# Kernel tuning notes

Measured on AMD Instinct MI355X. Metric: run time of the kernel, lower is better.

The kernel has to match this reference:

```python
import jax, jax.numpy as jnp
import numpy as np

EMB = 768
HEADS = 8
B, N = 8, 1024

def _ln(x, g, b, eps=1e-5):
    mu = jnp.mean(x, axis=-1, keepdims=True)
    var = jnp.mean(jnp.square(x - mu), axis=-1, keepdims=True)
    return (x - mu) * jax.lax.rsqrt(var + eps) * g + b

def setup_inputs() -> dict:
    key = jax.random.key(0)
    ks = jax.random.split(key, 8)
    s_in = 0.02
    return {
        "x": jax.random.normal(ks[0], (B, N, EMB), jnp.float32),
        "w_qkvr": jax.random.normal(ks[1], (EMB, 4 * EMB), jnp.float32) * s_in,
        "b_qkvr": jnp.zeros((4 * EMB,), jnp.float32),
        "w_proj": jax.random.normal(ks[2], (EMB, EMB), jnp.float32) * s_in,
        "b_proj": jnp.zeros((EMB,), jnp.float32),
        "ln1_g": jnp.ones((EMB,), jnp.float32),
        "ln1_b": jnp.zeros((EMB,), jnp.float32),
        "w_ff1": jax.random.normal(ks[3], (EMB, 4 * EMB), jnp.float32) * s_in,
        "b_ff1": jnp.zeros((4 * EMB,), jnp.float32),
        "w_ff2": jax.random.normal(ks[4], (4 * EMB, EMB), jnp.float32) * s_in,
        "b_ff2": jnp.zeros((EMB,), jnp.float32),
        "ln2_g": jnp.ones((EMB,), jnp.float32),
        "ln2_b": jnp.zeros((EMB,), jnp.float32),
    }

def reference(x, w_qkvr, b_qkvr, w_proj, b_proj, ln1_g, ln1_b,
              w_ff1, b_ff1, w_ff2, b_ff2, ln2_g, ln2_b):
    b, n, e = x.shape
    h = HEADS
    d = e // h
    # fused QKV+R projection; einops '(h d qkvr)' => qkvr is the INNERMOST factor
    qkvr = (x @ w_qkvr + b_qkvr).reshape(b, n, h, d, 4)
    qkvr = jnp.transpose(qkvr, (4, 0, 2, 1, 3))  # [4, b, h, n, d]
    q, k, v, r = qkvr[0], qkvr[1], qkvr[2], qkvr[3]
    energy = jnp.einsum('bhqd,bhkd->bhqk', q, k)
    # quirk: softmax of UNSCALED logits, then divide by sqrt(emb_size) AFTER
    att = jax.nn.softmax(energy, axis=-1) / jnp.sqrt(jnp.float32(e))
    out = jnp.einsum('bhqk,bhkd->bhqd', att, v)
    out = out * r  # elementwise r-gate
    out = jnp.transpose(out, (0, 2, 1, 3)).reshape(b, n, e)
    out = out @ w_proj + b_proj
    x1 = _ln(out + x, ln1_g, ln1_b)  # residual then post-LayerNorm
    ff = jax.nn.gelu(x1 @ w_ff1 + b_ff1, approximate=False) @ w_ff2 + b_ff2
    return _ln(ff + x1, ln2_g, ln2_b)
```

## Files before the change

kernel.cpp:

```cpp
#include <hip/hip_runtime.h>
#include <math.h>


typedef __bf16 bf16_t;
typedef __bf16 bf16x4 __attribute__((ext_vector_type(4)));
typedef __bf16 bf16x8 __attribute__((ext_vector_type(8)));
typedef float f32x4 __attribute__((ext_vector_type(4)));

#define EMB   768
#define HEADS 8
#define DHEAD 96
#define BATCH 8
#define SEQ   1024
#define ROWS  (BATCH * SEQ)
#define ACTN  ((size_t)ROWS * EMB)

__device__ __forceinline__ void load16_lds(const bf16_t* g, bf16_t* l) {
    __builtin_amdgcn_global_load_lds(
        (__attribute__((address_space(1))) unsigned int*)g,
        (__attribute__((address_space(3))) unsigned int*)l,
        16, 0, 0);
}


__device__ __forceinline__ void tile_transpose(
    const float* __restrict__ in, bf16_t* __restrict__ out,
    int K, int N, int n0, int k0, float (*t)[33], int tx, int ty0)
{
#pragma unroll
    for (int i = 0; i < 4; i++) {
        int ty = ty0 + 8 * i;
        t[ty][tx] = in[(size_t)(k0 + ty) * N + n0 + tx];
    }
    __syncthreads();
#pragma unroll
    for (int i = 0; i < 4; i++) {
        int ty = ty0 + 8 * i;
        out[(size_t)(n0 + ty) * K + k0 + tx] = (bf16_t)t[tx][ty];
    }
}

__global__ __launch_bounds__(256) void prep_kernel(
    const float* __restrict__ x, bf16_t* __restrict__ xb,
    const float* __restrict__ w_qkvr, bf16_t* __restrict__ wqkvrT,
    const float* __restrict__ w_proj, bf16_t* __restrict__ wprojT,
    const float* __restrict__ w_ff1, bf16_t* __restrict__ wff1T,
    const float* __restrict__ w_ff2, bf16_t* __restrict__ wff2T)
{
    __shared__ float t[32][33];
    int id = blockIdx.x;
    if (id < 768) {
        const int n4 = (int)(ACTN / 4);
        const int stride = 768 * 256;
        for (int i = id * 256 + threadIdx.x; i < n4; i += stride) {
            const float4 v = ((const float4*)x)[i];
            bf16x4 o;
            o[0] = (bf16_t)v.x; o[1] = (bf16_t)v.y;
            o[2] = (bf16_t)v.z; o[3] = (bf16_t)v.w;
            ((bf16x4*)xb)[i] = o;
        }
        return;
    }
    id -= 768;
    const int tx = threadIdx.x & 31, ty0 = threadIdx.x >> 5;
    if (id < 2304) {
        const int n0 = (id % 96) * 32, k0 = (id / 96) * 32;
        const int which = n0 / 768, hd0 = n0 % 768;
#pragma unroll
        for (int i = 0; i < 4; i++) {
            int ty = ty0 + 8 * i;
            t[ty][tx] = w_qkvr[(size_t)(k0 + ty) * 3072 + (hd0 + tx) * 4 + which];
        }
        __syncthreads();
#pragma unroll
        for (int i = 0; i < 4; i++) {
            int ty = ty0 + 8 * i;
            wqkvrT[(size_t)(n0 + ty) * 768 + k0 + tx] = (bf16_t)t[tx][ty];
        }
        return;
    }
    id -= 2304;
    if (id < 576) {
        tile_transpose(w_proj, wprojT, 768, 768, (id % 24) * 32, (id / 24) * 32, t, tx, ty0);
        return;
    }
    id -= 576;
    if (id < 2304) {
        tile_transpose(w_ff1, wff1T, 768, 3072, (id % 96) * 32, (id / 96) * 32, t, tx, ty0);
        return;
    }
    id -= 2304;
    {
        tile_transpose(w_ff2, wff2T, 3072, 768, (id % 24) * 32, (id / 24) * 32, t, tx, ty0);
    }
}


enum { EPI_QKVR = 0, EPI_PROJ = 1, EPI_GELU = 2, EPI_FF2 = 3 };

#define VMW6 asm volatile("s_waitcnt vmcnt(6)" ::: "memory")
#define VMW0 asm volatile("s_waitcnt vmcnt(0)" ::: "memory")
#define VMNONE do {} while (0)

#define RD8(KC, LB) do { \
    _Pragma("unroll") for (int u = 0; u < 4; u++) { \
        af[u]  = *reinterpret_cast<const bf16x8*>((LB) + aoff[KC][u]); \
        bfr[u] = *reinterpret_cast<const bf16x8*>((LB) + boff[KC][u]); \
    } \
} while (0)

#define MM16() do { \
    __builtin_amdgcn_s_setprio(1); \
    _Pragma("unroll") for (int tr = 0; tr < 4; tr++) \
        _Pragma("unroll") for (int tc = 0; tc < 4; tc++) \
            acc[tr][tc] = __builtin_amdgcn_mfma_f32_16x16x32_bf16( \
                af[tr], bfr[tc], acc[tr][tc], 0, 0, 0); \
    __builtin_amdgcn_s_setprio(0); \
} while (0)

#define STAGE6(DB) do { \
    bf16_t* db_ = lds + (DB) * 24576; \
    _Pragma("unroll") for (int i2 = 0; i2 < 4; i2++) { load16_lds(pa[i2], db_ + lA[i2]); pa[i2] += 64; } \
    _Pragma("unroll") for (int i2 = 0; i2 < 2; i2++) { load16_lds(pb[i2], db_ + lB[i2]); pb[i2] += 64; } \
} while (0)

#define TILE1(BUF, DOSTAGE, GATE, DOBAR) do { \
    const char* lb_ = (const char*)lds + (BUF) * 49152; \
    bf16x8 af[4], bfr[4]; \
    RD8(0, lb_); \
    if (DOSTAGE) STAGE6(((BUF) + 2) % 3); \
    MM16(); \
    RD8(1, lb_); \
    MM16(); \
    GATE; \
    if (DOBAR) { __builtin_amdgcn_sched_barrier(0); __builtin_amdgcn_s_barrier(); } \
} while (0)

template <int EPI, int KSTRIDE, int NKT, int NBX>
__global__ __launch_bounds__(512, 2) void gemmsb_kernel(
    const bf16_t* __restrict__ A,
    const bf16_t* __restrict__ BT,
    const float* __restrict__ bias,
    bf16_t* __restrict__ qo, bf16_t* __restrict__ ko,
    bf16_t* __restrict__ vTo, bf16_t* __restrict__ ro,
    const float* __restrict__ resid,
    float* __restrict__ outf,
    bf16_t* __restrict__ outb)
{
    __shared__ __align__(16) bf16_t lds[3 * 24576];

    const int tid  = threadIdx.x;
    const int wave = tid >> 6, lane = tid & 63;
    const int quad = lane >> 4, col16 = lane & 15;
    const int wrow = (wave >> 1) * 64, wcol = (wave & 1) * 64;

    const int cpx  = gridDim.x >> 3;
    const int id   = blockIdx.x;
    const int wgid = (id & 7) * cpx + (id >> 3);
    const int bx = wgid % NBX, by = wgid / NBX;
    const int m0 = by * 256, n0 = bx * 128;

    int aoff[2][4], boff[2][4];
#pragma unroll
    for (int kc = 0; kc < 2; kc++) {
#pragma unroll
        for (int u = 0; u < 4; u++) {
            const int R = wrow + u * 16 + col16;
            aoff[kc][u] = R * 128 + (((kc * 4 + quad) ^ (R & 7)) * 16);
            const int S = wcol + u * 16 + col16;
            boff[kc][u] = 32768 + S * 128 + (((kc * 4 + quad) ^ (S & 7)) * 16);
        }
    }

    const bf16_t* pa[4]; const bf16_t* pb[2];
    int lA[4], lB[2];
#pragma unroll
    for (int i = 0; i < 4; i++) {
        const int u = tid + 512 * i;
        const int r = u >> 3, j = (u & 7) ^ (r & 7);
        pa[i] = A + (size_t)(m0 + r) * KSTRIDE + j * 8;
        lA[i] = u * 8;
    }
#pragma unroll
    for (int i = 0; i < 2; i++) {
        const int u = tid + 512 * i;
        const int r = u >> 3, j = (u & 7) ^ (r & 7);
        pb[i] = BT + (size_t)(n0 + r) * KSTRIDE + j * 8;
        lB[i] = 16384 + u * 8;
    }

    f32x4 acc[4][4] = {};

    STAGE6(0); STAGE6(1);
    VMW6; __builtin_amdgcn_s_barrier();

#pragma unroll 1
    for (int tg = 0; tg < NKT / 3 - 1; ++tg) {
        TILE1(0, 1, VMW6, 1);
        TILE1(1, 1, VMW6, 1);
        TILE1(2, 1, VMW6, 1);
    }
    TILE1(0, 1, VMW6, 1);
    TILE1(1, 0, VMW0, 1);
    TILE1(2, 0, VMNONE, 0);

    if (EPI == EPI_QKVR) {
        const int whichb = bx / 6;
        if (whichb == 2) {
#pragma unroll
            for (int tr = 0; tr < 4; tr++) {
#pragma unroll
                for (int tc = 0; tc < 4; tc++) {
                    const int hd   = (bx % 6) * 128 + wcol + tc * 16 + col16;
                    const int head = hd / DHEAD, dd = hd % DHEAD;
                    const float bv = bias[hd * 4 + 2];
                    const int row0 = m0 + wrow + tr * 16 + quad * 4;
                    const int b = row0 >> 10, nn0 = row0 & 1023;
                    bf16x4 w;
#pragma unroll
                    for (int rg = 0; rg < 4; rg++) w[rg] = (bf16_t)(acc[tr][tc][rg] + bv);
                    *reinterpret_cast<bf16x4*>(
                        vTo + ((size_t)(b * HEADS + head) * DHEAD + dd) * SEQ + nn0) = w;
                }
            }
        } else {
            bf16_t* dst = (whichb == 0) ? qo : (whichb == 1) ? ko : ro;
#pragma unroll
            for (int tr = 0; tr < 4; tr++) {
#pragma unroll
                for (int tc = 0; tc < 4; tc++) {
                    const int hd   = (bx % 6) * 128 + wcol + tc * 16 + col16;
                    const int head = hd / DHEAD, dd = hd % DHEAD;
                    const float bv = bias[hd * 4 + whichb];
#pragma unroll
                    for (int rg = 0; rg < 4; rg++) {
                        const int row = m0 + wrow + tr * 16 + quad * 4 + rg;
                        const int b = row >> 10, nn = row & 1023;
                        dst[((size_t)(b * HEADS + head) * SEQ + nn) * DHEAD + dd] =
                            (bf16_t)(acc[tr][tc][rg] + bv);
                    }
                }
            }
        }
    } else {
#pragma unroll
        for (int tr = 0; tr < 4; tr++) {
#pragma unroll
            for (int tc = 0; tc < 4; tc++) {
#pragma unroll
                for (int rg = 0; rg < 4; rg++) {
                    const int row  = m0 + wrow + tr * 16 + quad * 4 + rg;
                    const int colg = n0 + wcol + tc * 16 + col16;
                    float v = acc[tr][tc][rg] + bias[colg];
                    if (EPI == EPI_PROJ || EPI == EPI_FF2) {
                        outf[(size_t)row * EMB + colg] = v + resid[(size_t)row * EMB + colg];
                    } else {
                        const float z = 1.5957691216057308f * v * (1.0f + 0.044715f * v * v);
                        const float g = v / (1.0f + __expf(-z));
                        outb[(size_t)row * 3072 + colg] = (bf16_t)g;
                    }
                }
            }
        }
    }
}


__global__ __launch_bounds__(256) void attn_kernel(
    const bf16_t* __restrict__ q, const bf16_t* __restrict__ k,
    const bf16_t* __restrict__ vT, const bf16_t* __restrict__ r,
    bf16_t* __restrict__ attn_out)
{
    __shared__ __align__(16) bf16_t Ks[64 * 96];
    __shared__ __align__(16) bf16_t Vs[96 * 64];
    __shared__ __align__(16) bf16_t P[4][16 * 72];

    const int tid = threadIdx.x, wave = tid >> 6, lane = tid & 63;
    const int quad = lane >> 4, col = lane & 15;
    const int bh = blockIdx.x & 63, qb = blockIdx.x >> 6;
    const int n0 = qb * 64 + wave * 16;
    const bf16_t* qp = q  + (size_t)bh * SEQ * DHEAD;
    const bf16_t* kb = k  + (size_t)bh * SEQ * DHEAD;
    const bf16_t* vb = vT + (size_t)bh * DHEAD * SEQ;
    bf16_t* Pw = P[wave];

    bf16x8 qf[3];
#pragma unroll
    for (int ks = 0; ks < 3; ks++)
        qf[ks] = *reinterpret_cast<const bf16x8*>(qp + (size_t)(n0 + col) * DHEAD + ks * 32 + quad * 8);

    const int u0 = tid, u1 = tid + 256, u2 = tid + 512;
    const int vf0 = u0 >> 3, vp0 = (u0 & 7) ^ (vf0 & 7);
    const int vf1 = u1 >> 3, vp1 = (u1 & 7) ^ (vf1 & 7);
    const int vf2 = u2 >> 3, vp2 = (u2 & 7) ^ (vf2 & 7);

    f32x4 O[6] = {};
    float lsum = 0.f;

    for (int ch = 0; ch < SEQ / 64; ch++) {
        const int kc0 = ch * 64;
        __syncthreads();
        const bf16_t* ksrc = kb + (size_t)kc0 * DHEAD;
        load16_lds(ksrc + u0 * 8, Ks + u0 * 8);
        load16_lds(ksrc + u1 * 8, Ks + u1 * 8);
        load16_lds(ksrc + u2 * 8, Ks + u2 * 8);
        load16_lds(vb + (size_t)vf0 * SEQ + kc0 + vp0 * 8, Vs + u0 * 8);
        load16_lds(vb + (size_t)vf1 * SEQ + kc0 + vp1 * 8, Vs + u1 * 8);
        load16_lds(vb + (size_t)vf2 * SEQ + kc0 + vp2 * 8, Vs + u2 * 8);
        __syncthreads();

        f32x4 s[4] = {};
#pragma unroll
        for (int ks = 0; ks < 3; ks++) {
#pragma unroll
            for (int h = 0; h < 4; h++) {
                bf16x8 kf = *reinterpret_cast<const bf16x8*>(Ks + (h * 16 + col) * DHEAD + ks * 32 + quad * 8);
                s[h] = __builtin_amdgcn_mfma_f32_16x16x32_bf16(kf, qf[ks], s[h], 0, 0, 0);
            }
        }
#pragma unroll
        for (int h = 0; h < 4; h++) {
            bf16x4 w;
#pragma unroll
            for (int rg = 0; rg < 4; rg++) {
                const float e = __expf(s[h][rg]);
                lsum += e;
                w[rg] = (bf16_t)e;
            }
            *reinterpret_cast<bf16x4*>(Pw + col * 72 + h * 16 + quad * 4) = w;
        }
        bf16x8 af0 = *reinterpret_cast<const bf16x8*>(Pw + col * 72 + quad * 8);
        bf16x8 af1 = *reinterpret_cast<const bf16x8*>(Pw + col * 72 + 32 + quad * 8);
#pragma unroll
        for (int tc = 0; tc < 6; tc++) {
            const int feat = tc * 16 + col;
            bf16x8 bv0 = *reinterpret_cast<const bf16x8*>(Vs + feat * 64 + ((quad)     ^ (col & 7)) * 8);
            bf16x8 bv1 = *reinterpret_cast<const bf16x8*>(Vs + feat * 64 + ((4 + quad) ^ (col & 7)) * 8);
            O[tc] = __builtin_amdgcn_mfma_f32_16x16x32_bf16(af0, bv0, O[tc], 0, 0, 0);
            O[tc] = __builtin_amdgcn_mfma_f32_16x16x32_bf16(af1, bv1, O[tc], 0, 0, 0);
        }
    }

    lsum += __shfl_xor(lsum, 16);
    lsum += __shfl_xor(lsum, 32);

    const float inv_sqrt_emb = 0.036084391824351615f;
    const int b = bh >> 3, h = bh & 7;
#pragma unroll
    for (int rg = 0; rg < 4; rg++) {
        const int nrow = quad * 4 + rg;
        const float lr = __shfl(lsum, nrow);
        const float scale = inv_sqrt_emb / lr;
        const int n = n0 + nrow;
#pragma unroll
        for (int tc = 0; tc < 6; tc++) {
            const int feat = tc * 16 + col;
            const float rv = (float)r[((size_t)bh * SEQ + n) * DHEAD + feat];
            attn_out[((size_t)(b * SEQ + n)) * EMB + h * DHEAD + feat] = (bf16_t)(O[tc][rg] * scale * rv);
        }
    }
}


__global__ __launch_bounds__(256) void ln_kernel(
    const float* __restrict__ in,
    const float* __restrict__ g, const float* __restrict__ b,
    float* __restrict__ y, bf16_t* __restrict__ yb)
{
    const int row = blockIdx.x * 4 + (threadIdx.x >> 6);
    const int lane = threadIdx.x & 63;
    const float4* rp = (const float4*)(in + (size_t)row * EMB);
    float4 v[3];
    float sum = 0.f;
#pragma unroll
    for (int i = 0; i < 3; i++) {
        float4 t = rp[lane + i * 64];
        v[i] = t;
        sum += t.x + t.y + t.z + t.w;
    }
#pragma unroll
    for (int off = 32; off; off >>= 1) sum += __shfl_xor(sum, off);
    const float mean = sum * (1.0f / 768.0f);
    float s2 = 0.f;
#pragma unroll
    for (int i = 0; i < 3; i++) {
        float dx = v[i].x - mean, dy = v[i].y - mean, dz = v[i].z - mean, dw = v[i].w - mean;
        s2 += dx * dx + dy * dy + dz * dz + dw * dw;
    }
#pragma unroll
    for (int off = 32; off; off >>= 1) s2 += __shfl_xor(s2, off);
    const float inv = rsqrtf(s2 * (1.0f / 768.0f) + 1e-5f);
    const float4* g4 = (const float4*)g;
    const float4* b4 = (const float4*)b;
#pragma unroll
    for (int i = 0; i < 3; i++) {
        const int c4 = lane + i * 64;
        const float4 gg = g4[c4], bb = b4[c4];
        float4 o;
        o.x = (v[i].x - mean) * inv * gg.x + bb.x;
        o.y = (v[i].y - mean) * inv * gg.y + bb.y;
        o.z = (v[i].z - mean) * inv * gg.z + bb.z;
        o.w = (v[i].w - mean) * inv * gg.w + bb.w;
        ((float4*)(y + (size_t)row * EMB))[c4] = o;
        if (yb) {
            bf16x4 ob;
            ob[0] = (bf16_t)o.x; ob[1] = (bf16_t)o.y; ob[2] = (bf16_t)o.z; ob[3] = (bf16_t)o.w;
            *reinterpret_cast<bf16x4*>(yb + (size_t)row * EMB + c4 * 4) = ob;
        }
    }
}


extern "C" void kernel_launch(void* const* d_in, const int* in_sizes, int n_in,
                              void* d_out, int out_size, void* d_ws, size_t ws_size,
                              hipStream_t stream)
{
    const float* x      = (const float*)d_in[0];
    const float* w_qkvr = (const float*)d_in[1];
    const float* b_qkvr = (const float*)d_in[2];
    const float* w_proj = (const float*)d_in[3];
    const float* b_proj = (const float*)d_in[4];
    const float* ln1_g  = (const float*)d_in[5];
    const float* ln1_b  = (const float*)d_in[6];
    const float* w_ff1  = (const float*)d_in[7];
    const float* b_ff1  = (const float*)d_in[8];
    const float* w_ff2  = (const float*)d_in[9];
    const float* b_ff2  = (const float*)d_in[10];
    const float* ln2_g  = (const float*)d_in[11];
    const float* ln2_b  = (const float*)d_in[12];
    float* out = (float*)d_out;

    char* ws = (char*)d_ws;
    size_t off = 0;
    auto alloc = [&](size_t bytes) {
        char* p = ws + off;
        off += (bytes + 255) & ~(size_t)255;
        return (void*)p;
    };
    bf16_t* wqkvrT  = (bf16_t*)alloc((size_t)3072 * 768 * 2);
    bf16_t* wprojT  = (bf16_t*)alloc((size_t)768 * 768 * 2);
    bf16_t* wff1T   = (bf16_t*)alloc((size_t)3072 * 768 * 2);
    bf16_t* wff2T   = (bf16_t*)alloc((size_t)768 * 3072 * 2);
    float*  x1f     = (float*)alloc(ACTN * 4);
    bf16_t* x1b     = (bf16_t*)alloc(ACTN * 2);
    bf16_t* ff1     = (bf16_t*)alloc((size_t)ROWS * 3072 * 2);
    bf16_t* xb      = (bf16_t*)alloc(ACTN * 2);
    bf16_t* qbuf    = (bf16_t*)alloc(ACTN * 2);
    bf16_t* kbuf    = (bf16_t*)alloc(ACTN * 2);
    bf16_t* vTbuf   = (bf16_t*)alloc(ACTN * 2);
    bf16_t* rbuf    = (bf16_t*)alloc(ACTN * 2);
    bf16_t* attn_o  = (bf16_t*)alloc(ACTN * 2);
    float*  res     = out;

    prep_kernel<<<8256, 256, 0, stream>>>(x, xb, w_qkvr, wqkvrT, w_proj, wprojT,
                                          w_ff1, wff1T, w_ff2, wff2T);

    gemmsb_kernel<EPI_QKVR, 768, 12, 24><<<768, 512, 0, stream>>>(
        xb, wqkvrT, b_qkvr, qbuf, kbuf, vTbuf, rbuf, nullptr, nullptr, nullptr);

    attn_kernel<<<dim3(SEQ / 64 * BATCH * HEADS), 256, 0, stream>>>(qbuf, kbuf, vTbuf, rbuf, attn_o);

    gemmsb_kernel<EPI_PROJ, 768, 12, 6><<<192, 512, 0, stream>>>(
        attn_o, wprojT, b_proj, nullptr, nullptr, nullptr, nullptr, x, res, nullptr);
    ln_kernel<<<2048, 256, 0, stream>>>(res, ln1_g, ln1_b, x1f, x1b);

    gemmsb_kernel<EPI_GELU, 768, 12, 24><<<768, 512, 0, stream>>>(
        x1b, wff1T, b_ff1, nullptr, nullptr, nullptr, nullptr, nullptr, nullptr, ff1);

    gemmsb_kernel<EPI_FF2, 3072, 48, 6><<<192, 512, 0, stream>>>(
        ff1, wff2T, b_ff2, nullptr, nullptr, nullptr, nullptr, x1f, res, nullptr);
    ln_kernel<<<2048, 256, 0, stream>>>(res, ln2_g, ln2_b, out, nullptr);

    (void)in_sizes; (void)n_in; (void)out_size; (void)ws_size;
}
```

Measured before the change: 358.1 us.

## Switch GEMM inner loop to 32x32x16 MFMA with k-major LDS layout

New measurement: 490.5 us. 1.37x slower.

```diff
diff --git a/kernel.cpp b/kernel.cpp
--- a/kernel.cpp
+++ b/kernel.cpp
@@ -6,6 +6,7 @@
 typedef __bf16 bf16x4 __attribute__((ext_vector_type(4)));
 typedef __bf16 bf16x8 __attribute__((ext_vector_type(8)));
 typedef float f32x4 __attribute__((ext_vector_type(4)));
+typedef float f32x16 __attribute__((ext_vector_type(16)));
 
 #define EMB   768
 #define HEADS 8
@@ -102,42 +103,44 @@
 #define VMW0 asm volatile("s_waitcnt vmcnt(0)" ::: "memory")
 #define VMNONE do {} while (0)
 
-#define RD8(KC, LB) do { \
-    _Pragma("unroll") for (int u = 0; u < 4; u++) { \
-        af[u]  = *reinterpret_cast<const bf16x8*>((LB) + aoff[KC][u]); \
-        bfr[u] = *reinterpret_cast<const bf16x8*>((LB) + boff[KC][u]); \
-    } \
-} while (0)
-
-#define MM16() do { \
-    __builtin_amdgcn_s_setprio(1); \
-    _Pragma("unroll") for (int tr = 0; tr < 4; tr++) \
-        _Pragma("unroll") for (int tc = 0; tc < 4; tc++) \
-            acc[tr][tc] = __builtin_amdgcn_mfma_f32_16x16x32_bf16( \
-                af[tr], bfr[tc], acc[tr][tc], 0, 0, 0); \
-    __builtin_amdgcn_s_setprio(0); \
-} while (0)
-
 #define STAGE6(DB) do { \
     bf16_t* db_ = lds + (DB) * 24576; \
     _Pragma("unroll") for (int i2 = 0; i2 < 4; i2++) { load16_lds(pa[i2], db_ + lA[i2]); pa[i2] += 64; } \
     _Pragma("unroll") for (int i2 = 0; i2 < 2; i2++) { load16_lds(pb[i2], db_ + lB[i2]); pb[i2] += 64; } \
 } while (0)
 
+#define HALF(KSA, KSB, LB, PRE) do { \
+    bf16x8 aA0 = *(const bf16x8*)((LB) + abase + (KSA) * 8192); \
+    bf16x8 aA1 = *(const bf16x8*)((LB) + abase + (KSA) * 8192 + 512); \
+    bf16x8 bA0 = *(const bf16x8*)((LB) + bbase + (KSA) * 4096); \
+    bf16x8 bA1 = *(const bf16x8*)((LB) + bbase + (KSA) * 4096 + 512); \
+    bf16x8 aB0 = *(const bf16x8*)((LB) + abase + (KSB) * 8192); \
+    bf16x8 aB1 = *(const bf16x8*)((LB) + abase + (KSB) * 8192 + 512); \
+    bf16x8 bB0 = *(const bf16x8*)((LB) + bbase + (KSB) * 4096); \
+    bf16x8 bB1 = *(const bf16x8*)((LB) + bbase + (KSB) * 4096 + 512); \
+    PRE; \
+    __builtin_amdgcn_s_setprio(1); \
+    acc[0][0] = __builtin_amdgcn_mfma_f32_32x32x16_bf16(aA0, bA0, acc[0][0], 0, 0, 0); \
+    acc[0][1] = __builtin_amdgcn_mfma_f32_32x32x16_bf16(aA0, bA1, acc[0][1], 0, 0, 0); \
+    acc[1][0] = __builtin_amdgcn_mfma_f32_32x32x16_bf16(aA1, bA0, acc[1][0], 0, 0, 0); \
+    acc[1][1] = __builtin_amdgcn_mfma_f32_32x32x16_bf16(aA1, bA1, acc[1][1], 0, 0, 0); \
+    acc[0][0] = __builtin_amdgcn_mfma_f32_32x32x16_bf16(aB0, bB0, acc[0][0], 0, 0, 0); \
+    acc[0][1] = __builtin_amdgcn_mfma_f32_32x32x16_bf16(aB0, bB1, acc[0][1], 0, 0, 0); \
+    acc[1][0] = __builtin_amdgcn_mfma_f32_32x32x16_bf16(aB1, bB0, acc[1][0], 0, 0, 0); \
+    acc[1][1] = __builtin_amdgcn_mfma_f32_32x32x16_bf16(aB1, bB1, acc[1][1], 0, 0, 0); \
+    __builtin_amdgcn_s_setprio(0); \
+} while (0)
+
 #define TILE1(BUF, DOSTAGE, GATE, DOBAR) do { \
     const char* lb_ = (const char*)lds + (BUF) * 49152; \
-    bf16x8 af[4], bfr[4]; \
-    RD8(0, lb_); \
-    if (DOSTAGE) STAGE6(((BUF) + 2) % 3); \
-    MM16(); \
-    RD8(1, lb_); \
-    MM16(); \
+    HALF(0, 1, lb_, if (DOSTAGE) STAGE6(((BUF) + 2) % 3)); \
+    HALF(2, 3, lb_, VMNONE); \
     GATE; \
     if (DOBAR) { __builtin_amdgcn_sched_barrier(0); __builtin_amdgcn_s_barrier(); } \
 } while (0)
 
 template <int EPI, int KSTRIDE, int NKT, int NBX>
-__global__ __launch_bounds__(512, 2) void gemmsb_kernel(
+__global__ __launch_bounds__(512, 2) void gemm32_kernel(
     const bf16_t* __restrict__ A,
     const bf16_t* __restrict__ BT,
     const float* __restrict__ bias,
@@ -151,7 +154,7 @@
 
     const int tid  = threadIdx.x;
     const int wave = tid >> 6, lane = tid & 63;
-    const int quad = lane >> 4, col16 = lane & 15;
+    const int ln = lane & 31, hi = lane >> 5;
     const int wrow = (wave >> 1) * 64, wcol = (wave & 1) * 64;
 
     const int cpx  = gridDim.x >> 3;
@@ -160,36 +163,25 @@
     const int bx = wgid % NBX, by = wgid / NBX;
     const int m0 = by * 256, n0 = bx * 128;
 
-    int aoff[2][4], boff[2][4];
-#pragma unroll
-    for (int kc = 0; kc < 2; kc++) {
-#pragma unroll
-        for (int u = 0; u < 4; u++) {
-            const int R = wrow + u * 16 + col16;
-            aoff[kc][u] = R * 128 + (((kc * 4 + quad) ^ (R & 7)) * 16);
-            const int S = wcol + u * 16 + col16;
-            boff[kc][u] = 32768 + S * 128 + (((kc * 4 + quad) ^ (S & 7)) * 16);
-        }
-    }
+    const int abase = (wrow + ln) * 16 + hi * 4096;
+    const int bbase = 32768 + (wcol + ln) * 16 + hi * 2048;
 
     const bf16_t* pa[4]; const bf16_t* pb[2];
     int lA[4], lB[2];
 #pragma unroll
     for (int i = 0; i < 4; i++) {
         const int u = tid + 512 * i;
-        const int r = u >> 3, j = (u & 7) ^ (r & 7);
-        pa[i] = A + (size_t)(m0 + r) * KSTRIDE + j * 8;
+        pa[i] = A + (size_t)(m0 + (u & 255)) * KSTRIDE + (u >> 8) * 8;
         lA[i] = u * 8;
     }
 #pragma unroll
     for (int i = 0; i < 2; i++) {
         const int u = tid + 512 * i;
-        const int r = u >> 3, j = (u & 7) ^ (r & 7);
-        pb[i] = BT + (size_t)(n0 + r) * KSTRIDE + j * 8;
+        pb[i] = BT + (size_t)(n0 + (u & 127)) * KSTRIDE + (u >> 7) * 8;
         lB[i] = 16384 + u * 8;
     }
 
-    f32x4 acc[4][4] = {};
+    f32x16 acc[2][2] = {};
 
     STAGE6(0); STAGE6(1);
     VMW6; __builtin_amdgcn_s_barrier();
@@ -208,17 +200,20 @@
         const int whichb = bx / 6;
         if (whichb == 2) {
 #pragma unroll
-            for (int tr = 0; tr < 4; tr++) {
-#pragma unroll
-                for (int tc = 0; tc < 4; tc++) {
-                    const int hd   = (bx % 6) * 128 + wcol + tc * 16 + col16;
-                    const int head = hd / DHEAD, dd = hd % DHEAD;
-                    const float bv = bias[hd * 4 + 2];
-                    const int row0 = m0 + wrow + tr * 16 + quad * 4;
+            for (int mb = 0; mb < 2; mb++)
+#pragma unroll
+            for (int nb = 0; nb < 2; nb++) {
+                const int hd   = (bx % 6) * 128 + wcol + nb * 32 + ln;
+                const int head = hd / DHEAD, dd = hd % DHEAD;
+                const float bv = bias[hd * 4 + 2];
+#pragma unroll
+                for (int g = 0; g < 4; g++) {
+                    const int row0 = m0 + wrow + mb * 32 + g * 8 + hi * 4;
                     const int b = row0 >> 10, nn0 = row0 & 1023;
                     bf16x4 w;
 #pragma unroll
-                    for (int rg = 0; rg < 4; rg++) w[rg] = (bf16_t)(acc[tr][tc][rg] + bv);
+                    for (int rg = 0; rg < 4; rg++)
+                        w[rg] = (bf16_t)(acc[mb][nb][g * 4 + rg] + bv);
                     *reinterpret_cast<bf16x4*>(
                         vTo + ((size_t)(b * HEADS + head) * DHEAD + dd) * SEQ + nn0) = w;
                 }
@@ -226,38 +221,42 @@
         } else {
             bf16_t* dst = (whichb == 0) ? qo : (whichb == 1) ? ko : ro;
 #pragma unroll
-            for (int tr = 0; tr < 4; tr++) {
-#pragma unroll
-                for (int tc = 0; tc < 4; tc++) {
-                    const int hd   = (bx % 6) * 128 + wcol + tc * 16 + col16;
-                    const int head = hd / DHEAD, dd = hd % DHEAD;
-                    const float bv = bias[hd * 4 + whichb];
+            for (int mb = 0; mb < 2; mb++)
+#pragma unroll
+            for (int nb = 0; nb < 2; nb++) {
+                const int hd   = (bx % 6) * 128 + wcol + nb * 32 + ln;
+                const int head = hd / DHEAD, dd = hd % DHEAD;
+                const float bv = bias[hd * 4 + whichb];
+#pragma unroll
+                for (int g = 0; g < 4; g++) {
 #pragma unroll
                     for (int rg = 0; rg < 4; rg++) {
-                        const int row = m0 + wrow + tr * 16 + quad * 4 + rg;
+                        const int row = m0 + wrow + mb * 32 + g * 8 + hi * 4 + rg;
                         const int b = row >> 10, nn = row & 1023;
                         dst[((size_t)(b * HEADS + head) * SEQ + nn) * DHEAD + dd] =
-                            (bf16_t)(acc[tr][tc][rg] + bv);
+                            (bf16_t)(acc[mb][nb][g * 4 + rg] + bv);
                     }
                 }
             }
         }
     } else {
 #pragma unroll
-        for (int tr = 0; tr < 4; tr++) {
-#pragma unroll
-            for (int tc = 0; tc < 4; tc++) {
+        for (int mb = 0; mb < 2; mb++)
+#pragma unroll
+        for (int nb = 0; nb < 2; nb++) {
+            const int colg = n0 + wcol + nb * 32 + ln;
+#pragma unroll
+            for (int g = 0; g < 4; g++) {
 #pragma unroll
                 for (int rg = 0; rg < 4; rg++) {
-                    const int row  = m0 + wrow + tr * 16 + quad * 4 + rg;
-                    const int colg = n0 + wcol + tc * 16 + col16;
-                    float v = acc[tr][tc][rg] + bias[colg];
+                    const int row = m0 + wrow + mb * 32 + g * 8 + hi * 4 + rg;
+                    float v = acc[mb][nb][g * 4 + rg] + bias[colg];
                     if (EPI == EPI_PROJ || EPI == EPI_FF2) {
                         outf[(size_t)row * EMB + colg] = v + resid[(size_t)row * EMB + colg];
                     } else {
                         const float z = 1.5957691216057308f * v * (1.0f + 0.044715f * v * v);
-                        const float g = v / (1.0f + __expf(-z));
-                        outb[(size_t)row * 3072 + colg] = (bf16_t)g;
+                        const float gl = v / (1.0f + __expf(-z));
+                        outb[(size_t)row * 3072 + colg] = (bf16_t)gl;
                     }
                 }
             }
@@ -455,19 +454,19 @@
     prep_kernel<<<8256, 256, 0, stream>>>(x, xb, w_qkvr, wqkvrT, w_proj, wprojT,
                                           w_ff1, wff1T, w_ff2, wff2T);
 
-    gemmsb_kernel<EPI_QKVR, 768, 12, 24><<<768, 512, 0, stream>>>(
+    gemm32_kernel<EPI_QKVR, 768, 12, 24><<<768, 512, 0, stream>>>(
         xb, wqkvrT, b_qkvr, qbuf, kbuf, vTbuf, rbuf, nullptr, nullptr, nullptr);
 
     attn_kernel<<<dim3(SEQ / 64 * BATCH * HEADS), 256, 0, stream>>>(qbuf, kbuf, vTbuf, rbuf, attn_o);
 
-    gemmsb_kernel<EPI_PROJ, 768, 12, 6><<<192, 512, 0, stream>>>(
+    gemm32_kernel<EPI_PROJ, 768, 12, 6><<<192, 512, 0, stream>>>(
         attn_o, wprojT, b_proj, nullptr, nullptr, nullptr, nullptr, x, res, nullptr);
     ln_kernel<<<2048, 256, 0, stream>>>(res, ln1_g, ln1_b, x1f, x1b);
 
-    gemmsb_kernel<EPI_GELU, 768, 12, 24><<<768, 512, 0, stream>>>(
+    gemm32_kernel<EPI_GELU, 768, 12, 24><<<768, 512, 0, stream>>>(
         x1b, wff1T, b_ff1, nullptr, nullptr, nullptr, nullptr, nullptr, nullptr, ff1);
 
-    gemmsb_kernel<EPI_FF2, 3072, 48, 6><<<192, 512, 0, stream>>>(
+    gemm32_kernel<EPI_FF2, 3072, 48, 6><<<192, 512, 0, stream>>>(
         ff1, wff2T, b_ff2, nullptr, nullptr, nullptr, nullptr, x1f, res, nullptr);
     ln_kernel<<<2048, 256, 0, stream>>>(res, ln2_g, ln2_b, out, nullptr);
 
```
